# Optimization experiments

Measured on AMD Instinct MI355X. Metric: run time of the kernel, lower is better.

The kernel has to match this reference:

```python
import jax, jax.numpy as jnp
import numpy as np


def setup_inputs() -> dict:
    key = jax.random.key(0)
    ks = jax.random.split(key, 7)
    B, S, D = 256, 1024, 128  # batch of sets, set size, n_input
    H = 256
    x = jax.random.normal(ks[0], (B, S, D), dtype=jnp.float32)
    # torch nn.Linear weights: [out_features, in_features], in = 2*layer_in
    W0 = jax.random.normal(ks[1], (H, 2 * D), dtype=jnp.float32) * 0.05
    b0 = jnp.zeros((H,), dtype=jnp.float32)
    W1 = jax.random.normal(ks[2], (H, 2 * H), dtype=jnp.float32) * 0.05
    b1 = jnp.zeros((H,), dtype=jnp.float32)
    W2 = jax.random.normal(ks[3], (H, 2 * H), dtype=jnp.float32) * 0.05
    b2 = jnp.zeros((H,), dtype=jnp.float32)
    return {"x": x, "W0": W0, "b0": b0, "W1": W1, "b1": b1, "W2": W2, "b2": b2}


def reference(x, W0, b0, W1, b1, W2, b2):
    # x: [B, S, D] batch of sets. Original loops over batch; we vmap.
    def apply_set(y):
        # y: [S, d]
        for W, b in ((W0, b0), (W1, b1), (W2, b2)):
            mean = jnp.mean(y, axis=0, keepdims=True)            # [1, d]
            mean = jnp.broadcast_to(mean, y.shape)               # [S, d]
            z = jnp.concatenate([y, mean], axis=1)               # [S, 2d]
            y = jnp.tanh(z @ W.T + b)                            # [S, out]
        return jnp.mean(y, axis=0)                               # [out]
    return jax.vmap(apply_set)(x)                                # [B, out]
```

## Files before the change

### kernel.cpp

```cpp
#include <hip/hip_runtime.h>

#define B_ 256
#define S_ 1024
#define D_ 128
#define H_ 256

typedef short short8 __attribute__((ext_vector_type(8)));
typedef float f32x4 __attribute__((ext_vector_type(4)));

__device__ unsigned short g_Wb0[H_ * D_];
__device__ unsigned short g_Wb1[H_ * H_];
__device__ unsigned short g_Wb2[H_ * H_];
__device__ float g_Wc0[H_ * D_];
__device__ float g_Wc1[H_ * H_];
__device__ float g_Wc2[H_ * H_];
__device__ float g_colsum1[B_ * H_];
__device__ float g_colsum2[B_ * H_];
__device__ float g_c0[B_ * H_];
__device__ float g_c1[B_ * H_];
__device__ float g_c2[B_ * H_];
__device__ unsigned short g_xb[(size_t)B_ * S_ * D_];

__device__ __forceinline__ unsigned short f2bf(float x) {
    union { float f; unsigned u; } v; v.f = x;
    unsigned r = v.u + 0x7FFFu + ((v.u >> 16) & 1u);
    return (unsigned short)(r >> 16);
}
__device__ __forceinline__ float bf2f(unsigned short h) {
    union { float f; unsigned u; } v; v.u = ((unsigned)h) << 16;
    return v.f;
}
__device__ __forceinline__ float fast_tanh(float x) {
    float e = __builtin_amdgcn_exp2f(x * 2.885390081777927f);
    float r = __builtin_amdgcn_rcpf(1.0f + e);
    return 1.0f - 2.0f * r;
}
__device__ __forceinline__ unsigned cvt_pk_bf16(float lo, float hi) {
    unsigned r;
    asm("v_cvt_pk_bf16_f32 %0, %1, %2" : "=v"(r) : "v"(lo), "v"(hi));
    return r;
}
__device__ __forceinline__ void gload_lds16(const unsigned short* g, unsigned short* l) {
    __builtin_amdgcn_global_load_lds(
        (const __attribute__((address_space(1))) void*)g,
        (__attribute__((address_space(3))) void*)l, 16, 0, 0);
}
__device__ __forceinline__ float row16_reduce_add(float v) {
    int s;
    s = __builtin_amdgcn_update_dpp(0, __builtin_bit_cast(int, v), 0x111, 0xF, 0xF, true);
    v += __builtin_bit_cast(float, s);
    s = __builtin_amdgcn_update_dpp(0, __builtin_bit_cast(int, v), 0x112, 0xF, 0xF, true);
    v += __builtin_bit_cast(float, s);
    s = __builtin_amdgcn_update_dpp(0, __builtin_bit_cast(int, v), 0x114, 0xF, 0xF, true);
    v += __builtin_bit_cast(float, s);
    s = __builtin_amdgcn_update_dpp(0, __builtin_bit_cast(int, v), 0x118, 0xF, 0xF, true);
    v += __builtin_bit_cast(float, s);
    return v;
}

__global__ __launch_bounds__(256) void prep_kernel(
    const float* __restrict__ W0, const float* __restrict__ W1,
    const float* __restrict__ W2)
{
    int i = blockIdx.x * 256 + threadIdx.x;
    const float* W; unsigned short* wb; float* wc; int kbits;
    if (i < H_ * D_) { W = W0; wb = g_Wb0; wc = g_Wc0; kbits = 7; }
    else {
        i -= H_ * D_;
        if (i < H_ * H_) { W = W1; wb = g_Wb1; wc = g_Wc1; kbits = 8; }
        else {
            i -= H_ * H_;
            if (i >= H_ * H_) return;
            W = W2; wb = g_Wb2; wc = g_Wc2; kbits = 8;
        }
    }
    const int K = 1 << kbits, KS = K >> 5;
    const int n = i >> kbits, k = i & (K - 1);
    const float a = W[n * 2 * K + k];
    const float b = W[n * 2 * K + K + k];
    const unsigned short hb = f2bf(a);
    const int w = n >> 5, cf = (n >> 4) & 1, l15 = n & 15;
    const int ks = k >> 5, quad = (k >> 3) & 3, e = k & 7;
    wb[(((w * 2 + cf) * KS + ks) * 64 + quad * 16 + l15) * 8 + e] = hb;
    wc[n * K + k] = b + (a - bf2f(hb));
}

__global__ __launch_bounds__(1024) void means0_kernel(
    const float* __restrict__ x, const float* __restrict__ b0)
{
    const int set = blockIdx.x, t = threadIdx.x;
    const int cg = t & 31, rg = t >> 5;
    const float* xs = x + (size_t)set * S_ * D_;
    unsigned short* xd = g_xb + (size_t)set * S_ * D_;
    const int slot = cg >> 1, halfsel = (cg & 1) * 4;
    f32x4 s = (f32x4){0.f, 0.f, 0.f, 0.f};
    #pragma unroll 8
    for (int i = 0; i < 32; ++i) {
        const int row = rg + i * 32;
        f32x4 v = *(const f32x4*)(xs + row * D_ + cg * 4);
        s += v;
        uint2 pv;
        pv.x = cvt_pk_bf16(v[0], v[1]);
        pv.y = cvt_pk_bf16(v[2], v[3]);
        *(uint2*)(&xd[row * D_ + ((slot ^ (row & 7)) * 8) + halfsel]) = pv;
    }
    __shared__ f32x4 red[32][32];
    __shared__ float m_lds[D_];
    red[rg][cg] = s;
    __syncthreads();
    if (t < 32) {
        f32x4 a = red[0][t];
        #pragma unroll
        for (int g = 1; g < 32; ++g) a += red[g][t];
        #pragma unroll
        for (int c = 0; c < 4; ++c) m_lds[t * 4 + c] = a[c] * (1.f / S_);
    }
    __syncthreads();
    if (t < H_) {
        const float* wr = g_Wc0 + t * D_;
        float acc = 0.f;
        #pragma unroll 4
        for (int k = 0; k < D_; k += 4) {
            f32x4 w = *(const f32x4*)(wr + k);
            #pragma unroll
            for (int c = 0; c < 4; ++c) acc += m_lds[k + c] * w[c];
        }
        g_c0[set * H_ + t] = b0[t] + acc;
    }
}

template <int L>
__global__ __launch_bounds__(256) void c_kernel(const float* __restrict__ bias)
{
    const int j = threadIdx.x, sg = blockIdx.x * 4;
    const float* Wc = (L == 1) ? g_Wc1 : g_Wc2;
    const float* ms = (L == 1) ? g_colsum1 : g_colsum2;
    float* dst = (L == 1) ? g_c1 : g_c2;
    __shared__ float m_lds[4][H_];
    for (int i = j; i < 4 * H_; i += 256)
        m_lds[i >> 8][i & (H_ - 1)] = ms[(sg + (i >> 8)) * H_ + (i & (H_ - 1))] * (1.f / S_);
    __syncthreads();
    const float* wr = Wc + j * H_;
    float a0 = 0.f, a1 = 0.f, a2 = 0.f, a3 = 0.f;
    #pragma unroll 4
    for (int k = 0; k < H_; k += 4) {
        f32x4 w = *(const f32x4*)(wr + k);
        #pragma unroll
        for (int c = 0; c < 4; ++c) {
            a0 += m_lds[0][k + c] * w[c];
            a1 += m_lds[1][k + c] * w[c];
            a2 += m_lds[2][k + c] * w[c];
            a3 += m_lds[3][k + c] * w[c];
        }
    }
    const float bb = bias[j];
    dst[(sg + 0) * H_ + j] = bb + a0;
    dst[(sg + 1) * H_ + j] = bb + a1;
    dst[(sg + 2) * H_ + j] = bb + a2;
    dst[(sg + 3) * H_ + j] = bb + a3;
}

template <int LAYER>
__global__ __launch_bounds__(512, 2) void layer_kernel(
    unsigned short* ybuf, float* __restrict__ out)
{
    constexpr int K  = (LAYER == 0) ? D_ : H_;
    constexpr int KS = K / 32;
    constexpr int NCH = (64 * K / 8) / 512;
    constexpr int NT = S_ / 64;
    const int set = blockIdx.x;
    const int t = threadIdx.x;
    const int lane = t & 63, wave = t >> 6;
    const int l15 = lane & 15, quad = lane >> 4;

    __shared__ __align__(16) unsigned short y_lds[2][64 * K];

    const unsigned short* Wb = (LAYER == 0) ? g_Wb0 : (LAYER == 1) ? g_Wb1 : g_Wb2;
    const float* cvec = (LAYER == 0) ? g_c0 : (LAYER == 1) ? g_c1 : g_c2;
    const unsigned short* ysrc = (LAYER == 0) ? g_xb + (size_t)set * S_ * D_
                                              : ybuf + (size_t)set * S_ * H_;
    unsigned short* ydst = ybuf + (size_t)set * S_ * H_;

    short8 wf[2][KS];
    {
        const unsigned short* wb = Wb + (wave * 2 * KS * 64 + lane) * 8;
        #pragma unroll
        for (int cf = 0; cf < 2; ++cf)
            #pragma unroll
            for (int ks = 0; ks < KS; ++ks)
                wf[cf][ks] = *(const short8*)(wb + (cf * KS + ks) * 512);
    }
    const float* cv = cvec + set * H_ + wave * 32 + quad * 4;
    f32x4 creg0 = *(const f32x4*)(cv);
    f32x4 creg1 = *(const f32x4*)(cv + 16);

    #pragma unroll
    for (int c = 0; c < NCH; ++c)
        gload_lds16(ysrc + (c * 512 + t) * 8, &y_lds[0][(c * 512 + t) * 8]);

    f32x4 cs0 = (f32x4){0.f, 0.f, 0.f, 0.f};
    f32x4 cs1 = (f32x4){0.f, 0.f, 0.f, 0.f};

    for (int tt = 0; tt < NT; ++tt) {
        const int buf = tt & 1;
        asm volatile("s_waitcnt vmcnt(0)" ::: "memory");
        __builtin_amdgcn_s_barrier();
        __builtin_amdgcn_sched_barrier(0);
        if (tt + 1 < NT) {
            const unsigned short* src = ysrc + (tt + 1) * 64 * K;
            #pragma unroll
            for (int c = 0; c < NCH; ++c)
                gload_lds16(src + (c * 512 + t) * 8, &y_lds[buf ^ 1][(c * 512 + t) * 8]);
        }
        const unsigned short* yl = y_lds[buf];
        #pragma unroll
        for (int rf = 0; rf < 4; ++rf) {
            short8 bfr[KS];
            #pragma unroll
            for (int ks = 0; ks < KS; ++ks)
                bfr[ks] = *(const short8*)(
                    &yl[(rf * 16 + l15) * K + (((ks * 4 + quad) ^ (l15 & 7)) * 8)]);
            f32x4 ac0 = (f32x4){0.f, 0.f, 0.f, 0.f};
            f32x4 ac1 = (f32x4){0.f, 0.f, 0.f, 0.f};
            #pragma unroll
            for (int ks = 0; ks < KS; ++ks) {
                ac0 = __builtin_amdgcn_mfma_f32_16x16x32_bf16(wf[0][ks], bfr[ks], ac0, 0, 0, 0);
                ac1 = __builtin_amdgcn_mfma_f32_16x16x32_bf16(wf[1][ks], bfr[ks], ac1, 0, 0, 0);
            }
            const int row = tt * 64 + rf * 16 + l15;
            f32x4 th0, th1;
            #pragma unroll
            for (int r = 0; r < 4; ++r) th0[r] = fast_tanh(ac0[r] + creg0[r]);
            #pragma unroll
            for (int r = 0; r < 4; ++r) th1[r] = fast_tanh(ac1[r] + creg1[r]);
            cs0 += th0; cs1 += th1;
            if (LAYER < 2) {
                const int slot0 = wave * 4 + (quad >> 1);
                const int slot1 = slot0 + 2;
                uint2 p0, p1;
                p0.x = cvt_pk_bf16(th0[0], th0[1]); p0.y = cvt_pk_bf16(th0[2], th0[3]);
                p1.x = cvt_pk_bf16(th1[0], th1[1]); p1.y = cvt_pk_bf16(th1[2], th1[3]);
                unsigned short* yr = ydst + row * H_ + (quad & 1) * 4;
                *(uint2*)(&yr[(slot0 ^ (row & 7)) * 8]) = p0;
                *(uint2*)(&yr[(slot1 ^ (row & 7)) * 8]) = p1;
            }
        }
    }

    #pragma unroll
    for (int r = 0; r < 4; ++r) {
        cs0[r] = row16_reduce_add(cs0[r]);
        cs1[r] = row16_reduce_add(cs1[r]);
    }
    if (l15 == 15) {
        const int col = wave * 32 + quad * 4;
        if (LAYER == 2) {
            f32x4 o0, o1;
            #pragma unroll
            for (int r = 0; r < 4; ++r) { o0[r] = cs0[r] * (1.f / S_); o1[r] = cs1[r] * (1.f / S_); }
            *(f32x4*)(&out[set * H_ + col]) = o0;
            *(f32x4*)(&out[set * H_ + col + 16]) = o1;
        } else if (LAYER == 1) {
            *(f32x4*)(&g_colsum2[set * H_ + col]) = cs0;
            *(f32x4*)(&g_colsum2[set * H_ + col + 16]) = cs1;
        } else {
            *(f32x4*)(&g_colsum1[set * H_ + col]) = cs0;
            *(f32x4*)(&g_colsum1[set * H_ + col + 16]) = cs1;
        }
    }
}

extern "C" void kernel_launch(void* const* d_in, const int* in_sizes, int n_in,
                              void* d_out, int out_size, void* d_ws, size_t ws_size,
                              hipStream_t stream) {
    (void)in_sizes; (void)n_in; (void)out_size; (void)ws_size;
    const float* x  = (const float*)d_in[0];
    const float* W0 = (const float*)d_in[1];
    const float* b0 = (const float*)d_in[2];
    const float* W1 = (const float*)d_in[3];
    const float* b1 = (const float*)d_in[4];
    const float* W2 = (const float*)d_in[5];
    const float* b2 = (const float*)d_in[6];
    float* out = (float*)d_out;
    unsigned short* ws = (unsigned short*)d_ws;

    prep_kernel<<<dim3(640), dim3(256), 0, stream>>>(W0, W1, W2);
    means0_kernel<<<dim3(256), dim3(1024), 0, stream>>>(x, b0);
    layer_kernel<0><<<dim3(256), dim3(512), 0, stream>>>(ws, out);
    c_kernel<1><<<dim3(64), dim3(256), 0, stream>>>(b1);
    layer_kernel<1><<<dim3(256), dim3(512), 0, stream>>>(ws, out);
    c_kernel<2><<<dim3(64), dim3(256), 0, stream>>>(b2);
    layer_kernel<2><<<dim3(256), dim3(512), 0, stream>>>(ws, out);
}
```

Measured before the change: 380.6 us.

## Fuse three layer kernels and mean-correction kernels into one per-set kernel

Replaces the three layer launches and two c_kernel launches with a single fused kernel per set. It computes the mean correction in-block from LDS column sums and switches to a triple-buffered LDS pipeline that prefetches two tiles ahead, waiting on partial vmcnt counts. Separate ping-pong global buffers hold intermediate activations. This removes four launch boundaries and the global colsum/c round-trips, at the cost of 96KB of LDS per block and fragile hand-tuned vmcnt accounting that includes the activation stores.

```diff
diff --git a/kernel.cpp b/kernel.cpp
--- a/kernel.cpp
+++ b/kernel.cpp
@@ -14,11 +14,7 @@
 __device__ float g_Wc0[H_ * D_];
 __device__ float g_Wc1[H_ * H_];
 __device__ float g_Wc2[H_ * H_];
-__device__ float g_colsum1[B_ * H_];
-__device__ float g_colsum2[B_ * H_];
 __device__ float g_c0[B_ * H_];
-__device__ float g_c1[B_ * H_];
-__device__ float g_c2[B_ * H_];
 __device__ unsigned short g_xb[(size_t)B_ * S_ * D_];
 
 __device__ __forceinline__ unsigned short f2bf(float x) {
@@ -44,6 +40,15 @@
     __builtin_amdgcn_global_load_lds(
         (const __attribute__((address_space(1))) void*)g,
         (__attribute__((address_space(3))) void*)l, 16, 0, 0);
+}
+template <int N>
+__device__ __forceinline__ void vwait() {
+    if constexpr (N == 0)       asm volatile("s_waitcnt vmcnt(0)" ::: "memory");
+    else if constexpr (N == 4)  asm volatile("s_waitcnt vmcnt(4)" ::: "memory");
+    else if constexpr (N == 8)  asm volatile("s_waitcnt vmcnt(8)" ::: "memory");
+    else if constexpr (N == 10) asm volatile("s_waitcnt vmcnt(10)" ::: "memory");
+    else if constexpr (N == 12) asm volatile("s_waitcnt vmcnt(12)" ::: "memory");
+    else static_assert(N < 0, "unsupported vmcnt");
 }
 __device__ __forceinline__ float row16_reduce_add(float v) {
     int s;
@@ -129,57 +134,36 @@
     }
 }
 
-template <int L>
-__global__ __launch_bounds__(256) void c_kernel(const float* __restrict__ bias)
-{
-    const int j = threadIdx.x, sg = blockIdx.x * 4;
-    const float* Wc = (L == 1) ? g_Wc1 : g_Wc2;
-    const float* ms = (L == 1) ? g_colsum1 : g_colsum2;
-    float* dst = (L == 1) ? g_c1 : g_c2;
-    __shared__ float m_lds[4][H_];
-    for (int i = j; i < 4 * H_; i += 256)
-        m_lds[i >> 8][i & (H_ - 1)] = ms[(sg + (i >> 8)) * H_ + (i & (H_ - 1))] * (1.f / S_);
-    __syncthreads();
-    const float* wr = Wc + j * H_;
-    float a0 = 0.f, a1 = 0.f, a2 = 0.f, a3 = 0.f;
-    #pragma unroll 4
-    for (int k = 0; k < H_; k += 4) {
-        f32x4 w = *(const f32x4*)(wr + k);
-        #pragma unroll
-        for (int c = 0; c < 4; ++c) {
-            a0 += m_lds[0][k + c] * w[c];
-            a1 += m_lds[1][k + c] * w[c];
-            a2 += m_lds[2][k + c] * w[c];
-            a3 += m_lds[3][k + c] * w[c];
-        }
-    }
-    const float bb = bias[j];
-    dst[(sg + 0) * H_ + j] = bb + a0;
-    dst[(sg + 1) * H_ + j] = bb + a1;
-    dst[(sg + 2) * H_ + j] = bb + a2;
-    dst[(sg + 3) * H_ + j] = bb + a3;
-}
-
-template <int LAYER>
-__global__ __launch_bounds__(512, 2) void layer_kernel(
-    unsigned short* ybuf, float* __restrict__ out)
-{
-    constexpr int K  = (LAYER == 0) ? D_ : H_;
-    constexpr int KS = K / 32;
+
+template <int K>
+__device__ __forceinline__ void stage_tile(
+    const unsigned short* __restrict__ ysrc, unsigned short* lds, int tile, int tid)
+{
     constexpr int NCH = (64 * K / 8) / 512;
-    constexpr int NT = S_ / 64;
-    const int set = blockIdx.x;
-    const int t = threadIdx.x;
-    const int lane = t & 63, wave = t >> 6;
+    const unsigned short* src = ysrc + tile * (64 * K);
+    unsigned short* dst = lds + (tile % 3) * (64 * K);
+    #pragma unroll
+    for (int c = 0; c < NCH; ++c)
+        gload_lds16(src + (c * 512 + tid) * 8, dst + (c * 512 + tid) * 8);
+}
+
+template <int K, bool STORES>
+__device__ __forceinline__ void run_layer(
+    const unsigned short* __restrict__ Wb,
+    const unsigned short* __restrict__ ysrc,
+    unsigned short* __restrict__ ydst,
+    unsigned short* lds,
+    const f32x4 creg0, const f32x4 creg1,
+    f32x4& cs0, f32x4& cs1)
+{
+    constexpr int KS  = K / 32;
+    constexpr int NCH = (64 * K / 8) / 512;
+    constexpr int WN  = NCH + (STORES ? 8 : 0);
+    constexpr int WT  = STORES ? 8 : 0;
+    constexpr int NT  = S_ / 64;
+    const int tid = threadIdx.x;
+    const int lane = tid & 63, wave = tid >> 6;
     const int l15 = lane & 15, quad = lane >> 4;
-
-    __shared__ __align__(16) unsigned short y_lds[2][64 * K];
-
-    const unsigned short* Wb = (LAYER == 0) ? g_Wb0 : (LAYER == 1) ? g_Wb1 : g_Wb2;
-    const float* cvec = (LAYER == 0) ? g_c0 : (LAYER == 1) ? g_c1 : g_c2;
-    const unsigned short* ysrc = (LAYER == 0) ? g_xb + (size_t)set * S_ * D_
-                                              : ybuf + (size_t)set * S_ * H_;
-    unsigned short* ydst = ybuf + (size_t)set * S_ * H_;
 
     short8 wf[2][KS];
     {
@@ -190,29 +174,12 @@
             for (int ks = 0; ks < KS; ++ks)
                 wf[cf][ks] = *(const short8*)(wb + (cf * KS + ks) * 512);
     }
-    const float* cv = cvec + set * H_ + wave * 32 + quad * 4;
-    f32x4 creg0 = *(const f32x4*)(cv);
-    f32x4 creg1 = *(const f32x4*)(cv + 16);
-
-    #pragma unroll
-    for (int c = 0; c < NCH; ++c)
-        gload_lds16(ysrc + (c * 512 + t) * 8, &y_lds[0][(c * 512 + t) * 8]);
-
-    f32x4 cs0 = (f32x4){0.f, 0.f, 0.f, 0.f};
-    f32x4 cs1 = (f32x4){0.f, 0.f, 0.f, 0.f};
+    cs0 = (f32x4){0.f, 0.f, 0.f, 0.f};
+    cs1 = (f32x4){0.f, 0.f, 0.f, 0.f};
+    __syncthreads();
 
     for (int tt = 0; tt < NT; ++tt) {
-        const int buf = tt & 1;
-        asm volatile("s_waitcnt vmcnt(0)" ::: "memory");
-        __builtin_amdgcn_s_barrier();
-        __builtin_amdgcn_sched_barrier(0);
-        if (tt + 1 < NT) {
-            const unsigned short* src = ysrc + (tt + 1) * 64 * K;
-            #pragma unroll
-            for (int c = 0; c < NCH; ++c)
-                gload_lds16(src + (c * 512 + t) * 8, &y_lds[buf ^ 1][(c * 512 + t) * 8]);
-        }
-        const unsigned short* yl = y_lds[buf];
+        const unsigned short* yl = lds + (tt % 3) * (64 * K);
         #pragma unroll
         for (int rf = 0; rf < 4; ++rf) {
             short8 bfr[KS];
@@ -234,7 +201,7 @@
             #pragma unroll
             for (int r = 0; r < 4; ++r) th1[r] = fast_tanh(ac1[r] + creg1[r]);
             cs0 += th0; cs1 += th1;
-            if (LAYER < 2) {
+            if (STORES) {
                 const int slot0 = wave * 4 + (quad >> 1);
                 const int slot1 = slot0 + 2;
                 uint2 p0, p1;
@@ -245,28 +212,100 @@
                 *(uint2*)(&yr[(slot1 ^ (row & 7)) * 8]) = p1;
             }
         }
-    }
+        __builtin_amdgcn_sched_barrier(0);
+        if (tt + 2 < NT)
+            stage_tile<K>(ysrc, lds, tt + 2, tid);
+        __builtin_amdgcn_sched_barrier(0);
+        if (tt < NT - 2)       vwait<WN>();
+        else if (tt == NT - 2) vwait<WT>();
+        __builtin_amdgcn_s_barrier();
+        __builtin_amdgcn_sched_barrier(0);
+    }
+}
+
+__device__ __forceinline__ void c_phase(
+    const float* __restrict__ Wc, const float* __restrict__ bias,
+    const float* colsum_lds, float* cpart, float* c_lds)
+{
+    const int tid = threadIdx.x;
+    const int j = tid >> 1, h = tid & 1;
+    const float* wr = Wc + j * H_ + h * 128;
+    float acc = 0.f;
+    #pragma unroll 4
+    for (int k = 0; k < 128; k += 4) {
+        f32x4 w = *(const f32x4*)(wr + k);
+        #pragma unroll
+        for (int c = 0; c < 4; ++c)
+            acc += colsum_lds[h * 128 + k + c] * w[c];
+    }
+    cpart[tid] = acc * (1.f / S_);
+    __syncthreads();
+    if (tid < H_) c_lds[tid] = bias[tid] + cpart[2 * tid] + cpart[2 * tid + 1];
+    __syncthreads();
+}
+
+__global__ __launch_bounds__(512, 2) void fused_kernel(
+    const float* __restrict__ b1, const float* __restrict__ b2,
+    unsigned short* __restrict__ yA, unsigned short* __restrict__ yB,
+    float* __restrict__ out)
+{
+    __shared__ __align__(16) unsigned short y_lds[3 * 64 * H_];
+    __shared__ float colsum_lds[H_];
+    __shared__ float cpart[512];
+    __shared__ float c_lds[H_];
+    const int set = blockIdx.x;
+    const int tid = threadIdx.x;
+    const int lane = tid & 63, wave = tid >> 6;
+    const int l15 = lane & 15, quad = lane >> 4;
+    const int col = wave * 32 + quad * 4;
+
+    const unsigned short* x0 = g_xb + (size_t)set * S_ * D_;
+    unsigned short* ya = yA + (size_t)set * S_ * H_;
+    unsigned short* yb = yB + (size_t)set * S_ * H_;
+    f32x4 cs0, cs1, creg0, creg1;
+
+    stage_tile<D_>(x0, y_lds, 0, tid);
+    stage_tile<D_>(x0, y_lds, 1, tid);
+    creg0 = *(const f32x4*)(g_c0 + set * H_ + col);
+    creg1 = *(const f32x4*)(g_c0 + set * H_ + col + 16);
+    run_layer<D_, true>(g_Wb0, x0, ya, y_lds, creg0, creg1, cs0, cs1);
+    __syncthreads();
 
     #pragma unroll
-    for (int r = 0; r < 4; ++r) {
-        cs0[r] = row16_reduce_add(cs0[r]);
-        cs1[r] = row16_reduce_add(cs1[r]);
-    }
+    for (int r = 0; r < 4; ++r) { cs0[r] = row16_reduce_add(cs0[r]); cs1[r] = row16_reduce_add(cs1[r]); }
+    if (l15 == 15) { *(f32x4*)&colsum_lds[col] = cs0; *(f32x4*)&colsum_lds[col + 16] = cs1; }
+    stage_tile<H_>(ya, y_lds, 0, tid);
+    stage_tile<H_>(ya, y_lds, 1, tid);
+    asm volatile("s_waitcnt lgkmcnt(0)" ::: "memory");
+    __builtin_amdgcn_s_barrier();
+    c_phase(g_Wc1, b1, colsum_lds, cpart, c_lds);
+    creg0 = *(const f32x4*)&c_lds[col];
+    creg1 = *(const f32x4*)&c_lds[col + 16];
+
+    run_layer<H_, true>(g_Wb1, ya, yb, y_lds, creg0, creg1, cs0, cs1);
+    __syncthreads();
+
+    #pragma unroll
+    for (int r = 0; r < 4; ++r) { cs0[r] = row16_reduce_add(cs0[r]); cs1[r] = row16_reduce_add(cs1[r]); }
+    if (l15 == 15) { *(f32x4*)&colsum_lds[col] = cs0; *(f32x4*)&colsum_lds[col + 16] = cs1; }
+    stage_tile<H_>(yb, y_lds, 0, tid);
+    stage_tile<H_>(yb, y_lds, 1, tid);
+    asm volatile("s_waitcnt lgkmcnt(0)" ::: "memory");
+    __builtin_amdgcn_s_barrier();
+    c_phase(g_Wc2, b2, colsum_lds, cpart, c_lds);
+    creg0 = *(const f32x4*)&c_lds[col];
+    creg1 = *(const f32x4*)&c_lds[col + 16];
+
+    run_layer<H_, false>(g_Wb2, yb, yb, y_lds, creg0, creg1, cs0, cs1);
+
+    #pragma unroll
+    for (int r = 0; r < 4; ++r) { cs0[r] = row16_reduce_add(cs0[r]); cs1[r] = row16_reduce_add(cs1[r]); }
     if (l15 == 15) {
-        const int col = wave * 32 + quad * 4;
-        if (LAYER == 2) {
-            f32x4 o0, o1;
-            #pragma unroll
-            for (int r = 0; r < 4; ++r) { o0[r] = cs0[r] * (1.f / S_); o1[r] = cs1[r] * (1.f / S_); }
-            *(f32x4*)(&out[set * H_ + col]) = o0;
-            *(f32x4*)(&out[set * H_ + col + 16]) = o1;
-        } else if (LAYER == 1) {
-            *(f32x4*)(&g_colsum2[set * H_ + col]) = cs0;
-            *(f32x4*)(&g_colsum2[set * H_ + col + 16]) = cs1;
-        } else {
-            *(f32x4*)(&g_colsum1[set * H_ + col]) = cs0;
-            *(f32x4*)(&g_colsum1[set * H_ + col + 16]) = cs1;
-        }
+        f32x4 o0, o1;
+        #pragma unroll
+        for (int r = 0; r < 4; ++r) { o0[r] = cs0[r] * (1.f / S_); o1[r] = cs1[r] * (1.f / S_); }
+        *(f32x4*)(&out[set * H_ + col]) = o0;
+        *(f32x4*)(&out[set * H_ + col + 16]) = o1;
     }
 }
 
@@ -282,13 +321,10 @@
     const float* W2 = (const float*)d_in[5];
     const float* b2 = (const float*)d_in[6];
     float* out = (float*)d_out;
-    unsigned short* ws = (unsigned short*)d_ws;
+    unsigned short* yA = (unsigned short*)d_ws;
+    unsigned short* yB = yA + (size_t)B_ * S_ * H_;
 
     prep_kernel<<<dim3(640), dim3(256), 0, stream>>>(W0, W1, W2);
     means0_kernel<<<dim3(256), dim3(1024), 0, stream>>>(x, b0);
-    layer_kernel<0><<<dim3(256), dim3(512), 0, stream>>>(ws, out);
-    c_kernel<1><<<dim3(64), dim3(256), 0, stream>>>(b1);
-    layer_kernel<1><<<dim3(256), dim3(512), 0, stream>>>(ws, out);
-    c_kernel<2><<<dim3(64), dim3(256), 0, stream>>>(b2);
-    layer_kernel<2><<<dim3(256), dim3(512), 0, stream>>>(ws, out);
-}
+    fused_kernel<<<dim3(256), dim3(512), 0, stream>>>(b1, b2, yA, yB, out);
+}
```

After: 365.8 us. 1.04x faster.
